# Kernel tuning notes

Measured on AMD Instinct MI355X. Metric: run time of the kernel, lower is better.

## Reference

```python
import jax, jax.numpy as jnp
import numpy as np
import math

H = 768
NH = 12
DK = H // NH
EPS = 1e-12

def gelu(x):
    return 0.5 * x * (1 + jnp.tanh(math.sqrt(2 / math.pi) * (x + 0.044715 * x ** 3)))

def layernorm(x, w, b):
    u = x.mean(-1, keepdims=True)
    s = ((x - u) ** 2).mean(-1, keepdims=True)
    return w * (x - u) / jnp.sqrt(s + EPS) + b

def setup_inputs() -> dict:
    key = jax.random.key(0)
    ks = jax.random.split(key, 12)
    B, S = 4, 2048
    std = 1.0 / math.sqrt(H)
    inp = {
        'x': jax.random.normal(ks[0], (B, S, H), jnp.float32),
        'mask': jax.random.randint(ks[1], (B, S), 0, 2, jnp.int32),
        'wq': jax.random.normal(ks[2], (H, H), jnp.float32) * std,
        'wk': jax.random.normal(ks[3], (H, H), jnp.float32) * std,
        'wv': jax.random.normal(ks[4], (H, H), jnp.float32) * std,
        'wo': jax.random.normal(ks[5], (H, H), jnp.float32) * std,
        'wo_b': jnp.zeros((H,), jnp.float32),
        'w1': jax.random.normal(ks[6], (H, 4 * H), jnp.float32) * std,
        'w1_b': jnp.zeros((4 * H,), jnp.float32),
        'w2': jax.random.normal(ks[7], (4 * H, H), jnp.float32) * (0.5 / math.sqrt(H)),
        'w2_b': jnp.zeros((H,), jnp.float32),
        'ln1_w': jnp.ones((H,), jnp.float32),
        'ln1_b': jnp.zeros((H,), jnp.float32),
        'ln2_w': jnp.ones((H,), jnp.float32),
        'ln2_b': jnp.zeros((H,), jnp.float32),
    }
    return inp

def reference(x, mask, wq, wk, wv, wo, wo_b, w1, w1_b, w2, w2_b, ln1_w, ln1_b, ln2_w, ln2_b):
    B, S, _ = x.shape
    # --- attention sublayer (pre-LN, residual) ---
    y = layernorm(x, ln1_w, ln1_b)
    q = (y @ wq).reshape(B, S, NH, DK).transpose(0, 2, 1, 3)
    k = (y @ wk).reshape(B, S, NH, DK).transpose(0, 2, 1, 3)
    v = (y @ wv).reshape(B, S, NH, DK).transpose(0, 2, 1, 3)
    scores = jnp.einsum('bhqd,bhkd->bhqk', q, k) / math.sqrt(DK)
    m2 = (mask[:, :, None] * mask[:, None, :])[:, None, :, :]  # [B,1,S,S]
    scores = jnp.where(m2 == 0, jnp.float32(-1e9), scores)
    p = jax.nn.softmax(scores, axis=-1)
    ctx = jnp.einsum('bhqk,bhkd->bhqd', p, v).transpose(0, 2, 1, 3).reshape(B, S, H)
    x = x + ctx @ wo + wo_b
    # --- FFN sublayer ---
    y2 = layernorm(x, ln2_w, ln2_b)
    x = x + gelu(y2 @ w1 + w1_b) @ w2 + w2_b
    return x
```

## Files before the change

kernel.cpp:

```cpp
#include <hip/hip_runtime.h>
#include <hip/hip_bf16.h>

#define HD   768
#define BSZ  4
#define SEQ  2048
#define NTOK (BSZ*SEQ)
#define NHD  12
#define DKD  64

typedef __bf16 bf16_t;
typedef __bf16 bf16x8 __attribute__((ext_vector_type(8)));
typedef __bf16 bf16x4 __attribute__((ext_vector_type(4)));
typedef float  f32x4  __attribute__((ext_vector_type(4)));

__device__ __forceinline__ void async16(const void* g, void* l) {
    __builtin_amdgcn_global_load_lds(
        (const __attribute__((address_space(1))) unsigned int*)g,
        (__attribute__((address_space(3))) unsigned int*)l, 16, 0, 0);
}

__global__ __launch_bounds__(256) void wconv_kernel(
    const float* __restrict__ in, bf16_t* __restrict__ out, int K, int N)
{
    __shared__ float tile[32][33];
    const int k0 = blockIdx.y * 32, n0 = blockIdx.x * 32;
    const int t = threadIdx.x, r = t >> 5, c = t & 31;
#pragma unroll
    for (int j = 0; j < 4; j++)
        tile[r + 8*j][c] = in[(size_t)(k0 + r + 8*j) * N + n0 + c];
    __syncthreads();
#pragma unroll
    for (int j = 0; j < 4; j++)
        out[(size_t)(n0 + r + 8*j) * K + k0 + c] = (bf16_t)tile[c][r + 8*j];
}

__global__ __launch_bounds__(256) void mbias_kernel(
    const int* __restrict__ mask, float* __restrict__ mb)
{
    const int i = blockIdx.x * 256 + threadIdx.x;
    mb[i] = mask[i] ? 0.f : -1e9f;
}

__global__ __launch_bounds__(256) void ln_kernel(
    const float* __restrict__ x, const float* __restrict__ gw,
    const float* __restrict__ gb, bf16_t* __restrict__ y)
{
    const int row = blockIdx.x, t = threadIdx.x;
    const float* xr = x + (size_t)row * HD;
    float v0 = xr[t], v1 = xr[t + 256], v2 = xr[t + 512];
    float s1 = v0 + v1 + v2;
    float s2 = v0*v0 + v1*v1 + v2*v2;
#pragma unroll
    for (int m = 1; m < 64; m <<= 1) {
        s1 += __shfl_xor(s1, m);
        s2 += __shfl_xor(s2, m);
    }
    __shared__ float red[8];
    const int w = t >> 6, l = t & 63;
    if (l == 0) { red[w] = s1; red[4 + w] = s2; }
    __syncthreads();
    s1 = red[0] + red[1] + red[2] + red[3];
    s2 = red[4] + red[5] + red[6] + red[7];
    float mean = s1 * (1.f/HD);
    float var  = fmaxf(s2 * (1.f/HD) - mean*mean, 0.f);
    float rstd = rsqrtf(var + 1e-12f);
    bf16_t* yr = y + (size_t)row * HD;
    yr[t]       = (bf16_t)(gw[t]      * (v0 - mean) * rstd + gb[t]);
    yr[t + 256] = (bf16_t)(gw[t + 256]* (v1 - mean) * rstd + gb[t + 256]);
    yr[t + 512] = (bf16_t)(gw[t + 512]* (v2 - mean) * rstd + gb[t + 512]);
}

template<int EPI>
__global__ __launch_bounds__(256) void gemm_bt(
    const bf16_t* __restrict__ A, const bf16_t* __restrict__ BT,
    const float* __restrict__ bias, const float* __restrict__ resid,
    void* __restrict__ outv, int M, int N, int K, int ldo)
{
    __shared__ __align__(16) unsigned char lds[16384];
    const int t = threadIdx.x;
    const int w = t >> 6, l = t & 63;
    const int wr = w >> 1, wc = w & 1;
    const int lr = l & 15, lg = l >> 4;
    const int m0 = blockIdx.y * 128, n0 = blockIdx.x * 128;

    const bf16_t* a_src = A  + (size_t)(m0 + (t >> 2)) * K + (t & 3) * 8;
    const bf16_t* b_src = BT + (size_t)(n0 + (t >> 2)) * K + (t & 3) * 8;
    f32x4 acc[4][4] = {};

    for (int kt = 0; kt < K; kt += 32) {
        __syncthreads();
        async16(a_src + kt,                 lds + t*16);
        async16(a_src + (size_t)64*K + kt,  lds + 4096 + t*16);
        async16(b_src + kt,                 lds + 8192 + t*16);
        async16(b_src + (size_t)64*K + kt,  lds + 12288 + t*16);
        __syncthreads();
        bf16x8 af[4], bfr[4];
#pragma unroll
        for (int n = 0; n < 4; n++)
            bfr[n] = *(const bf16x8*)(lds + 8192 + (wc*64 + n*16 + lr)*64 + lg*16);
#pragma unroll
        for (int m = 0; m < 4; m++)
            af[m] = *(const bf16x8*)(lds + (wr*64 + m*16 + lr)*64 + lg*16);
#pragma unroll
        for (int m = 0; m < 4; m++)
#pragma unroll
            for (int n = 0; n < 4; n++)
                acc[m][n] = __builtin_amdgcn_mfma_f32_16x16x32_bf16(af[m], bfr[n], acc[m][n], 0, 0, 0);
    }

#pragma unroll
    for (int m = 0; m < 4; m++) {
#pragma unroll
        for (int n = 0; n < 4; n++) {
#pragma unroll
            for (int i = 0; i < 4; i++) {
                const int gr = m0 + wr*64 + m*16 + lg*4 + i;
                const int gc = n0 + wc*64 + n*16 + lr;
                float v = acc[m][n][i];
                if constexpr (EPI == 0) {
                    ((bf16_t*)outv)[(size_t)gr * ldo + gc] = (bf16_t)v;
                } else if constexpr (EPI == 1) {
                    ((float*)outv)[(size_t)gr * ldo + gc] =
                        v + bias[gc] + resid[(size_t)gr * ldo + gc];
                } else {
                    v += bias[gc];
                    float u = 0.7978845608028654f * (v + 0.044715f * v * v * v);
                    float g = 0.5f * v * (1.f + tanhf(u));
                    ((bf16_t*)outv)[(size_t)gr * ldo + gc] = (bf16_t)g;
                }
            }
        }
    }
}

__global__ __launch_bounds__(256) void vtrans_kernel(
    const bf16_t* __restrict__ qkv, bf16_t* __restrict__ vt)
{
    const int bh = blockIdx.y, b = bh / NHD, h = bh % NHD;
    const int s0 = blockIdx.x * 64;
    __shared__ bf16_t tile[64][72];
    const int t = threadIdx.x;
    {
        const int r = t >> 2, c0 = (t & 3) * 16;
        const bf16_t* src = qkv + (size_t)(b*SEQ + s0 + r) * 2304 + 1536 + h*64 + c0;
#pragma unroll
        for (int j = 0; j < 16; j++) tile[r][c0 + j] = src[j];
    }
    __syncthreads();
    {
        const int d = t >> 2, j0 = (t & 3) * 16;
        bf16_t* dst = vt + ((size_t)bh*64 + d) * SEQ + s0 + j0;
#pragma unroll
        for (int j = 0; j < 16; j++) dst[j] = tile[j0 + j][d];
    }
}

__global__ __launch_bounds__(256) void attn_kernel(
    const bf16_t* __restrict__ qkv, const bf16_t* __restrict__ vt,
    const int* __restrict__ mask, const float* __restrict__ mbias,
    bf16_t* __restrict__ ctx)
{
    __shared__ __align__(16) unsigned char lds[32768];
    const int bh = blockIdx.y, b = bh / NHD, h = bh % NHD;
    const int t = threadIdx.x, w = t >> 6, l = t & 63;
    const int lr = l & 15, lg = l >> 4;
    const int q0 = blockIdx.x * 128 + w * 32;
    const int swz = (lr & 7) << 4;

    bf16x8 qf[2][2];
#pragma unroll
    for (int r = 0; r < 2; r++)
#pragma unroll
        for (int ks = 0; ks < 2; ks++)
            qf[r][ks] = *(const bf16x8*)(qkv + (size_t)(b*SEQ + q0 + r*16 + lr)*2304
                                         + h*64 + ks*32 + lg*8);
    int mq[2];
#pragma unroll
    for (int r = 0; r < 2; r++)
        mq[r] = mask[b*SEQ + q0 + r*16 + lr];

    float mrow[2] = { -INFINITY, -INFINITY };
    float lsum[2] = { 0.f, 0.f };
    f32x4 accO[2][4] = {};

    for (int kt = 0; kt < SEQ; kt += 64) {
        __syncthreads();
#pragma unroll
        for (int i2 = 0; i2 < 2; i2++) {
            const int c = i2*256 + t;
            const int row = c >> 3;
            const int scol = ((c & 7) ^ (row & 7)) * 8;
            async16(qkv + (size_t)(b*SEQ + kt + row)*2304 + 768 + h*64 + scol,
                    lds + c*16);
        }
#pragma unroll
        for (int i2 = 0; i2 < 2; i2++) {
            const int c = i2*256 + t;
            const int row = c >> 3;
            const int scol = ((c & 7) ^ (row & 7)) * 8;
            async16(vt + ((size_t)bh*64 + row)*SEQ + kt + scol,
                    lds + 8192 + c*16);
        }
        f32x4 mb[4];
#pragma unroll
        for (int n = 0; n < 4; n++)
            mb[n] = *(const f32x4*)(mbias + (size_t)b*SEQ + kt + n*16 + lg*4);
        __syncthreads();

        bf16x8 kf[4][2];
#pragma unroll
        for (int n = 0; n < 4; n++)
#pragma unroll
            for (int ks = 0; ks < 2; ks++)
                kf[n][ks] = *(const bf16x8*)(lds + (n*16 + lr)*128
                                             + ((ks*64 + lg*16) ^ swz));
        f32x4 accS[4][2] = {};
        __builtin_amdgcn_s_setprio(1);
#pragma unroll
        for (int n = 0; n < 4; n++)
#pragma unroll
            for (int r = 0; r < 2; r++)
#pragma unroll
                for (int ks = 0; ks < 2; ks++)
                    accS[n][r] = __builtin_amdgcn_mfma_f32_16x16x32_bf16(
                        kf[n][ks], qf[r][ks], accS[n][r], 0, 0, 0);
        __builtin_amdgcn_s_setprio(0);

#pragma unroll
        for (int r = 0; r < 2; r++) {
            f32x4 sl[4];
#pragma unroll
            for (int n = 0; n < 4; n++)
#pragma unroll
                for (int i = 0; i < 4; i++)
                    sl[n][i] = mq[r] ? (accS[n][r][i] * 0.125f + mb[n][i]) : -1e9f;
            float px = -INFINITY;
#pragma unroll
            for (int n = 0; n < 4; n++)
                px = fmaxf(px, fmaxf(fmaxf(sl[n][0], sl[n][1]),
                                     fmaxf(sl[n][2], sl[n][3])));
            px = fmaxf(px, __shfl_xor(px, 16));
            px = fmaxf(px, __shfl_xor(px, 32));
            const float mold = mrow[r];
            if (!__all(px <= mold + 8.f)) {
                const float mnew = fmaxf(mold, px);
                const float sc = __expf(mold - mnew);
                lsum[r] *= sc;
#pragma unroll
                for (int dn = 0; dn < 4; dn++) accO[r][dn] *= sc;
                mrow[r] = mnew;
            }
            const float m = mrow[r];
            float ps = 0.f;
#pragma unroll
            for (int n = 0; n < 4; n++) {
                bf16x4 pk;
#pragma unroll
                for (int i = 0; i < 4; i++) {
                    float pv = __expf(sl[n][i] - m);
                    ps += pv;
                    pk[i] = (bf16_t)pv;
                }
                *(bf16x4*)(lds + 16384 + w*4096 + (r*16 + lr)*128
                           + ((n*32 + lg*8) ^ swz)) = pk;
            }
            ps += __shfl_xor(ps, 16);
            ps += __shfl_xor(ps, 32);
            lsum[r] += ps;
        }

        bf16x8 vf[4][2], pf[2][2];
#pragma unroll
        for (int dn = 0; dn < 4; dn++)
#pragma unroll
            for (int ks = 0; ks < 2; ks++)
                vf[dn][ks] = *(const bf16x8*)(lds + 8192 + (dn*16 + lr)*128
                                              + ((ks*64 + lg*16) ^ swz));
#pragma unroll
        for (int r = 0; r < 2; r++)
#pragma unroll
            for (int ks = 0; ks < 2; ks++)
                pf[r][ks] = *(const bf16x8*)(lds + 16384 + w*4096 + (r*16 + lr)*128
                                             + ((ks*64 + lg*16) ^ swz));
        __builtin_amdgcn_s_setprio(1);
#pragma unroll
        for (int r = 0; r < 2; r++)
#pragma unroll
            for (int dn = 0; dn < 4; dn++)
#pragma unroll
                for (int ks = 0; ks < 2; ks++)
                    accO[r][dn] = __builtin_amdgcn_mfma_f32_16x16x32_bf16(
                        vf[dn][ks], pf[r][ks], accO[r][dn], 0, 0, 0);
        __builtin_amdgcn_s_setprio(0);
    }

#pragma unroll
    for (int r = 0; r < 2; r++) {
        const float inv = 1.f / lsum[r];
#pragma unroll
        for (int dn = 0; dn < 4; dn++) {
            bf16x4 ov;
#pragma unroll
            for (int i = 0; i < 4; i++)
                ov[i] = (bf16_t)(accO[r][dn][i] * inv);
            *(bf16x4*)(ctx + (size_t)(b*SEQ + q0 + r*16 + lr)*HD
                       + h*64 + dn*16 + lg*4) = ov;
        }
    }
}

extern "C" void kernel_launch(void* const* d_in, const int* in_sizes, int n_in,
                              void* d_out, int out_size, void* d_ws, size_t ws_size,
                              hipStream_t stream)
{
    const float* x     = (const float*)d_in[0];
    const int*   mask  = (const int*)  d_in[1];
    const float* wq    = (const float*)d_in[2];
    const float* wk    = (const float*)d_in[3];
    const float* wv    = (const float*)d_in[4];
    const float* wo    = (const float*)d_in[5];
    const float* wo_b  = (const float*)d_in[6];
    const float* w1    = (const float*)d_in[7];
    const float* w1_b  = (const float*)d_in[8];
    const float* w2    = (const float*)d_in[9];
    const float* w2_b  = (const float*)d_in[10];
    const float* ln1_w = (const float*)d_in[11];
    const float* ln1_b = (const float*)d_in[12];
    const float* ln2_w = (const float*)d_in[13];
    const float* ln2_b = (const float*)d_in[14];

    unsigned char* ws = (unsigned char*)d_ws;
    size_t o = 0;
    auto alloc = [&](size_t bytes) {
        size_t r = o; o += (bytes + 255) & ~(size_t)255; return r;
    };
    bf16_t* wqkvT = (bf16_t*)(ws + alloc((size_t)2304*768*2));
    bf16_t* woT   = (bf16_t*)(ws + alloc((size_t)768*768*2));
    bf16_t* w1T   = (bf16_t*)(ws + alloc((size_t)3072*768*2));
    bf16_t* w2T   = (bf16_t*)(ws + alloc((size_t)768*3072*2));
    bf16_t* y     = (bf16_t*)(ws + alloc((size_t)NTOK*HD*2));
    float*  x1    = (float*) (ws + alloc((size_t)NTOK*HD*4));
    bf16_t* ctx   = (bf16_t*)(ws + alloc((size_t)NTOK*HD*2));
    float*  mbias = (float*) (ws + alloc((size_t)NTOK*4));
    bf16_t* qkv   = (bf16_t*)(ws + alloc((size_t)NTOK*2304*2));
    bf16_t* vt    = (bf16_t*)(ws + alloc((size_t)48*64*SEQ*2));
    bf16_t* hbuf  = qkv;
    (void)in_sizes; (void)n_in; (void)out_size; (void)ws_size;

    wconv_kernel<<<dim3(24,24),256,0,stream>>>(wq, wqkvT,                 768, 768);
    wconv_kernel<<<dim3(24,24),256,0,stream>>>(wk, wqkvT + 768*768,       768, 768);
    wconv_kernel<<<dim3(24,24),256,0,stream>>>(wv, wqkvT + 2*768*768,     768, 768);
    wconv_kernel<<<dim3(24,24),256,0,stream>>>(wo, woT,                   768, 768);
    wconv_kernel<<<dim3(96,24),256,0,stream>>>(w1, w1T,                   768, 3072);
    wconv_kernel<<<dim3(24,96),256,0,stream>>>(w2, w2T,                   3072, 768);
    mbias_kernel<<<32,256,0,stream>>>(mask, mbias);

    ln_kernel<<<NTOK,256,0,stream>>>(x, ln1_w, ln1_b, y);
    gemm_bt<0><<<dim3(18,64),256,0,stream>>>(y, wqkvT, nullptr, nullptr, qkv,
                                             NTOK, 2304, 768, 2304);
    vtrans_kernel<<<dim3(32,48),256,0,stream>>>(qkv, vt);
    attn_kernel<<<dim3(16,48),256,0,stream>>>(qkv, vt, mask, mbias, ctx);
    gemm_bt<1><<<dim3(6,64),256,0,stream>>>(ctx, woT, wo_b, x, x1,
                                            NTOK, 768, 768, 768);
    ln_kernel<<<NTOK,256,0,stream>>>(x1, ln2_w, ln2_b, y);
    gemm_bt<2><<<dim3(24,64),256,0,stream>>>(y, w1T, w1_b, nullptr, hbuf,
                                             NTOK, 3072, 768, 3072);
    gemm_bt<1><<<dim3(6,64),256,0,stream>>>(hbuf, w2T, w2_b, x1, d_out,
                                            NTOK, 768, 3072, 768);
}
```

Before: 502.3 us.

## Multi-buffer GEMM and attention LDS loads and remap workgroups across XCDs

The GEMM now prefetches K-tiles two steps ahead into a triple-buffered LDS ring with explicit vmcnt waits, replacing the two full barriers per iteration. The attention kernel double-buffers its K/V tiles so the next tile's async loads overlap the current compute. Both kernels remap block indices so that neighbouring tiles land on the same XCD, which is meant to improve L2 reuse. The GELU tanh is rewritten as a sigmoid-style exp form. The larger LDS footprint (48KB) may lower occupancy, and the block remap assumes the grid size divides by 8.

```diff
diff --git a/kernel.cpp b/kernel.cpp
--- a/kernel.cpp
+++ b/kernel.cpp
@@ -76,36 +76,64 @@
     const float* __restrict__ bias, const float* __restrict__ resid,
     void* __restrict__ outv, int M, int N, int K, int ldo)
 {
-    __shared__ __align__(16) unsigned char lds[16384];
+    __shared__ __align__(16) unsigned char lds[49152];
     const int t = threadIdx.x;
     const int w = t >> 6, l = t & 63;
     const int wr = w >> 1, wc = w & 1;
     const int lr = l & 15, lg = l >> 4;
-    const int m0 = blockIdx.y * 128, n0 = blockIdx.x * 128;
+    const int nwg = gridDim.x * gridDim.y;
+    int flat = blockIdx.y * gridDim.x + blockIdx.x;
+    flat = (flat & 7) * (nwg >> 3) + (flat >> 3);
+    const int bx = flat % gridDim.x, by = flat / gridDim.x;
+    const int m0 = by * 128, n0 = bx * 128;
 
     const bf16_t* a_src = A  + (size_t)(m0 + (t >> 2)) * K + (t & 3) * 8;
     const bf16_t* b_src = BT + (size_t)(n0 + (t >> 2)) * K + (t & 3) * 8;
     f32x4 acc[4][4] = {};
 
-    for (int kt = 0; kt < K; kt += 32) {
-        __syncthreads();
-        async16(a_src + kt,                 lds + t*16);
-        async16(a_src + (size_t)64*K + kt,  lds + 4096 + t*16);
-        async16(b_src + kt,                 lds + 8192 + t*16);
-        async16(b_src + (size_t)64*K + kt,  lds + 12288 + t*16);
-        __syncthreads();
+    auto stage = [&](int kt, int buf) {
+        unsigned char* d = lds + buf * 16384 + t * 16;
+        async16(a_src + kt,                 d);
+        async16(a_src + (size_t)64*K + kt,  d + 4096);
+        async16(b_src + kt,                 d + 8192);
+        async16(b_src + (size_t)64*K + kt,  d + 12288);
+    };
+
+    const int nt = K >> 5;
+    stage(0, 0);
+    stage(32, 1);
+    asm volatile("s_waitcnt vmcnt(4)" ::: "memory");
+    __builtin_amdgcn_s_barrier();
+
+    int cur = 0;
+    for (int it = 0; it < nt; ++it) {
+        const bool pre = (it + 2 < nt);
+        if (pre) {
+            int b2 = cur + 2; if (b2 >= 3) b2 -= 3;
+            stage((it + 2) << 5, b2);
+        }
+        const unsigned char* bufp = lds + cur * 16384;
         bf16x8 af[4], bfr[4];
 #pragma unroll
         for (int n = 0; n < 4; n++)
-            bfr[n] = *(const bf16x8*)(lds + 8192 + (wc*64 + n*16 + lr)*64 + lg*16);
+            bfr[n] = *(const bf16x8*)(bufp + 8192 + (wc*64 + n*16 + lr)*64 + lg*16);
 #pragma unroll
         for (int m = 0; m < 4; m++)
-            af[m] = *(const bf16x8*)(lds + (wr*64 + m*16 + lr)*64 + lg*16);
+            af[m] = *(const bf16x8*)(bufp + (wr*64 + m*16 + lr)*64 + lg*16);
+        __builtin_amdgcn_s_setprio(1);
 #pragma unroll
         for (int m = 0; m < 4; m++)
 #pragma unroll
             for (int n = 0; n < 4; n++)
                 acc[m][n] = __builtin_amdgcn_mfma_f32_16x16x32_bf16(af[m], bfr[n], acc[m][n], 0, 0, 0);
+        __builtin_amdgcn_s_setprio(0);
+        if (it + 1 < nt) {
+            asm volatile("s_waitcnt lgkmcnt(0)" ::: "memory");
+            if (pre) asm volatile("s_waitcnt vmcnt(4)" ::: "memory");
+            else     asm volatile("s_waitcnt vmcnt(0)" ::: "memory");
+            __builtin_amdgcn_s_barrier();
+        }
+        cur = (cur + 1 == 3) ? 0 : cur + 1;
     }
 
 #pragma unroll
@@ -125,7 +153,7 @@
                 } else {
                     v += bias[gc];
                     float u = 0.7978845608028654f * (v + 0.044715f * v * v * v);
-                    float g = 0.5f * v * (1.f + tanhf(u));
+                    float g = v / (1.f + __expf(-2.f * u));
                     ((bf16_t*)outv)[(size_t)gr * ldo + gc] = (bf16_t)g;
                 }
             }
@@ -160,11 +188,14 @@
     const int* __restrict__ mask, const float* __restrict__ mbias,
     bf16_t* __restrict__ ctx)
 {
-    __shared__ __align__(16) unsigned char lds[32768];
-    const int bh = blockIdx.y, b = bh / NHD, h = bh % NHD;
+    __shared__ __align__(16) unsigned char lds[49152];
     const int t = threadIdx.x, w = t >> 6, l = t & 63;
     const int lr = l & 15, lg = l >> 4;
-    const int q0 = blockIdx.x * 128 + w * 32;
+    int flat = blockIdx.y * 16 + blockIdx.x;
+    flat = (flat & 7) * 96 + (flat >> 3);
+    const int bh = flat >> 4, qt = flat & 15;
+    const int b = bh / NHD, h = bh % NHD;
+    const int q0 = qt * 128 + w * 32;
     const int swz = (lr & 7) << 4;
 
     bf16x8 qf[2][2];
@@ -183,36 +214,38 @@
     float lsum[2] = { 0.f, 0.f };
     f32x4 accO[2][4] = {};
 
-    for (int kt = 0; kt < SEQ; kt += 64) {
-        __syncthreads();
+    auto stage_kv = [&](int kt, int buf) {
+        unsigned char* d = lds + buf * 16384;
 #pragma unroll
         for (int i2 = 0; i2 < 2; i2++) {
             const int c = i2*256 + t;
             const int row = c >> 3;
             const int scol = ((c & 7) ^ (row & 7)) * 8;
             async16(qkv + (size_t)(b*SEQ + kt + row)*2304 + 768 + h*64 + scol,
-                    lds + c*16);
-        }
-#pragma unroll
-        for (int i2 = 0; i2 < 2; i2++) {
-            const int c = i2*256 + t;
-            const int row = c >> 3;
-            const int scol = ((c & 7) ^ (row & 7)) * 8;
+                    d + c*16);
             async16(vt + ((size_t)bh*64 + row)*SEQ + kt + scol,
-                    lds + 8192 + c*16);
-        }
+                    d + 8192 + c*16);
+        }
+    };
+
+    stage_kv(0, 0);
+    __syncthreads();
+
+    int cur = 0;
+    for (int kt = 0; kt < SEQ; kt += 64) {
+        if (kt + 64 < SEQ) stage_kv(kt + 64, cur ^ 1);
         f32x4 mb[4];
 #pragma unroll
         for (int n = 0; n < 4; n++)
             mb[n] = *(const f32x4*)(mbias + (size_t)b*SEQ + kt + n*16 + lg*4);
-        __syncthreads();
+        const unsigned char* bufp = lds + cur * 16384;
 
         bf16x8 kf[4][2];
 #pragma unroll
         for (int n = 0; n < 4; n++)
 #pragma unroll
             for (int ks = 0; ks < 2; ks++)
-                kf[n][ks] = *(const bf16x8*)(lds + (n*16 + lr)*128
+                kf[n][ks] = *(const bf16x8*)(bufp + (n*16 + lr)*128
                                              + ((ks*64 + lg*16) ^ swz));
         f32x4 accS[4][2] = {};
         __builtin_amdgcn_s_setprio(1);
@@ -261,7 +294,7 @@
                     ps += pv;
                     pk[i] = (bf16_t)pv;
                 }
-                *(bf16x4*)(lds + 16384 + w*4096 + (r*16 + lr)*128
+                *(bf16x4*)(lds + 32768 + w*4096 + (r*16 + lr)*128
                            + ((n*32 + lg*8) ^ swz)) = pk;
             }
             ps += __shfl_xor(ps, 16);
@@ -274,13 +307,13 @@
         for (int dn = 0; dn < 4; dn++)
 #pragma unroll
             for (int ks = 0; ks < 2; ks++)
-                vf[dn][ks] = *(const bf16x8*)(lds + 8192 + (dn*16 + lr)*128
+                vf[dn][ks] = *(const bf16x8*)(bufp + 8192 + (dn*16 + lr)*128
                                               + ((ks*64 + lg*16) ^ swz));
 #pragma unroll
         for (int r = 0; r < 2; r++)
 #pragma unroll
             for (int ks = 0; ks < 2; ks++)
-                pf[r][ks] = *(const bf16x8*)(lds + 16384 + w*4096 + (r*16 + lr)*128
+                pf[r][ks] = *(const bf16x8*)(lds + 32768 + w*4096 + (r*16 + lr)*128
                                              + ((ks*64 + lg*16) ^ swz));
         __builtin_amdgcn_s_setprio(1);
 #pragma unroll
@@ -292,6 +325,9 @@
                     accO[r][dn] = __builtin_amdgcn_mfma_f32_16x16x32_bf16(
                         vf[dn][ks], pf[r][ks], accO[r][dn], 0, 0, 0);
         __builtin_amdgcn_s_setprio(0);
+
+        __syncthreads();
+        cur ^= 1;
     }
 
 #pragma unroll
```

Measured after the change: 435.0 us. -13.4%, faster.
